# Kernel optimization log

Measured on AMD Instinct MI355X. Metric: run time of the kernel, lower is better.

The kernel has to match this reference:

```python
import jax, jax.numpy as jnp
import numpy as np

B, D_IN, D_F = 4096, 1024, 256   # batch, extractor input dim, feature dim
M, K = 10, 8                      # n_mixtures, n_components per mixture
LOG2PI = float(np.log(2.0 * np.pi))


def setup_inputs() -> dict:
    key = jax.random.key(0)
    k0, k1, k2, k3, k4 = jax.random.split(key, 5)
    x = jax.random.normal(k0, (B, D_IN), jnp.float32)
    W = jax.random.normal(k1, (D_IN, D_F), jnp.float32) / np.sqrt(D_IN)
    b = jnp.zeros((D_F,), jnp.float32)
    means = jax.random.normal(k2, (M, K, D_F), jnp.float32)
    # full covariance parameter; tril is taken in forward; +I keeps the
    # Cholesky-factor diagonal positive, as torch MultivariateNormal requires
    covs = jax.random.normal(k3, (M, K, D_F, D_F), jnp.float32) * 0.01
    covs = covs + jnp.eye(D_F, dtype=jnp.float32)
    weights = jax.random.normal(k4, (M, K), jnp.float32)
    return {"x": x, "W": W, "b": b, "means": means, "covs": covs, "weights": weights}


def reference(x, W, b, means, covs, weights):
    # extractor: Linear + ReLU -> [B, D_F]
    feats = jax.nn.relu(x @ W + b)
    # scale_tril = tril(cov) for every (mixture, component): [M, K, D_F, D_F]
    L = jnp.tril(covs)
    # diff between every feature vector and every component mean: [M, K, B, D_F]
    diff = feats[None, None, :, :] - means[:, :, None, :]
    # batched triangular solve L z = diff^T -> z: [M, K, D_F, B]
    z = jax.scipy.linalg.solve_triangular(L, jnp.swapaxes(diff, -1, -2), lower=True)
    quad = jnp.sum(z * z, axis=-2)  # Mahalanobis term: [M, K, B]
    logdet = jnp.sum(jnp.log(jnp.diagonal(L, axis1=-2, axis2=-1)), axis=-1)  # [M, K]
    logp = -0.5 * (quad + D_F * LOG2PI) - logdet[..., None]  # MVN log_prob: [M, K, B]
    # per-mixture softmax over component weights, multiply into log-probs
    w = jax.nn.softmax(weights, axis=-1)  # [M, K]
    mix = w[..., None] * logp             # [M, K, B]
    # GMM returns [B, K]; DeepGMM stacks over mixtures and transposes -> [B, M, K]
    return jnp.transpose(mix, (2, 0, 1))
```

## Files before the change

kernel.cpp:

```cpp
#include <hip/hip_runtime.h>

#define B_N 4096
#define D_IN 1024
#define D_F 256
#define MK 80
#define LOG2PI 1.8378770664093453f
#define XP_S 72

typedef float f32x4 __attribute__((ext_vector_type(4)));
typedef short bf16x8 __attribute__((ext_vector_type(8)));
typedef float float4_ __attribute__((ext_vector_type(4)));
typedef unsigned int u32x4 __attribute__((ext_vector_type(4)));
typedef unsigned short u16x8 __attribute__((ext_vector_type(8)));

__device__ __forceinline__ unsigned short f2bf(float f) {
    unsigned u = __float_as_uint(f);
    u += 0x7fffu + ((u >> 16) & 1u);
    return (unsigned short)(u >> 16);
}
__device__ __forceinline__ float bf2f(unsigned short h) {
    return __uint_as_float(((unsigned)h) << 16);
}
__device__ __forceinline__ void gload_lds16(const void* g, void* l) {
    __builtin_amdgcn_global_load_lds((const __attribute__((address_space(1))) void*)g,
                                     (__attribute__((address_space(3))) void*)l, 16, 0, 0);
}
__device__ __forceinline__ bf16x8 pack8(float4_ a, float4_ b) {
    bf16x8 r;
    r[0] = (short)f2bf(a.x); r[1] = (short)f2bf(a.y);
    r[2] = (short)f2bf(a.z); r[3] = (short)f2bf(a.w);
    r[4] = (short)f2bf(b.x); r[5] = (short)f2bf(b.y);
    r[6] = (short)f2bf(b.z); r[7] = (short)f2bf(b.w);
    return r;
}

__global__ __launch_bounds__(256) void k_pre(const float* __restrict__ W,
                                             const float* __restrict__ covs,
                                             const float* __restrict__ wts,
                                             unsigned short* __restrict__ wt,
                                             float* __restrict__ wmix,
                                             float* __restrict__ ldet,
                                             unsigned short* __restrict__ covsb,
                                             float* __restrict__ dvec) {
    int bx = blockIdx.x, tid = threadIdx.x;
    if (bx < 64) {
        __shared__ unsigned short t[64][65];
        int k0 = (bx >> 2) * 64, n0 = (bx & 3) * 64;
        int r = tid / 64, c = tid % 64;
        #pragma unroll
        for (int rr = r; rr < 64; rr += 4)
            t[rr][c] = f2bf(W[(size_t)(k0 + rr) * D_F + n0 + c]);
        __syncthreads();
        #pragma unroll
        for (int rr = r; rr < 64; rr += 4)
            wt[(size_t)(n0 + rr) * D_IN + k0 + c] = t[c][rr];
    } else if (bx < 144) {
        if (tid < 64) {
            int mk = bx - 64;
            int l = tid;
            const float* Lm = covs + (size_t)mk * D_F * D_F;
            float s = 0.0f;
            for (int i = l; i < D_F; i += 64) s += logf(Lm[(size_t)i * D_F + i]);
            for (int off = 32; off; off >>= 1) s += __shfl_down(s, off);
            if (l == 0) {
                ldet[mk] = s;
                int m = mk / 8, k = mk % 8;
                float mx = -1e30f;
                for (int j = 0; j < 8; j++) mx = fmaxf(mx, wts[m * 8 + j]);
                float sum = 0.0f;
                for (int j = 0; j < 8; j++) sum += expf(wts[m * 8 + j] - mx);
                wmix[mk] = expf(wts[m * 8 + k] - mx) / sum;
            }
        }
    } else if (bx < 224) {
        int mk = bx - 144;
        const float* Cm = covs + (size_t)mk * D_F * D_F;
        unsigned short* Cb = covsb + (size_t)mk * 10 * 4096;
        #pragma unroll
        for (int I = 1; I < 4; ++I)
            for (int K = 0; K < I; ++K) {
                int idx = (I * (I - 1)) / 2 + K;
                for (int t4 = tid; t4 < 1024; t4 += 256) {
                    int r = t4 >> 4, kq = t4 & 15;
                    float4_ v = *(const float4_*)&Cm[(size_t)(I * 64 + r) * D_F
                                                     + K * 64 + kq * 4];
                    ushort4 o;
                    o.x = f2bf(v.x); o.y = f2bf(v.y); o.z = f2bf(v.z); o.w = f2bf(v.w);
                    *(ushort4*)&Cb[(size_t)idx * 4096 + r * 64 + kq * 4] = o;
                }
            }
    } else {
        int mk = bx - 224;
        const float* Cm = covs + (size_t)mk * D_F * D_F;
        unsigned short* Cb = covsb + (size_t)mk * 10 * 4096;
        __shared__ float rl[256];
        rl[tid] = 1.0f / Cm[(size_t)tid * D_F + tid];
        __syncthreads();
        dvec[mk * 256 + tid] = rl[tid];
        #pragma unroll
        for (int I = 0; I < 4; ++I) {
            for (int t4 = tid; t4 < 1024; t4 += 256) {
                int r = t4 >> 4, kq = t4 & 15;
                float4_ v = *(const float4_*)&Cm[(size_t)(I * 64 + r) * D_F
                                                 + I * 64 + kq * 4];
                float ri = rl[I * 64 + r];
                int base = kq * 4;
                ushort4 o;
                o.x = (base     < r) ? f2bf(v.x * ri) : (unsigned short)0;
                o.y = (base + 1 < r) ? f2bf(v.y * ri) : (unsigned short)0;
                o.z = (base + 2 < r) ? f2bf(v.z * ri) : (unsigned short)0;
                o.w = (base + 3 < r) ? f2bf(v.w * ri) : (unsigned short)0;
                *(ushort4*)&Cb[(size_t)(6 + I) * 4096 + r * 64 + base] = o;
            }
        }
    }
}

__global__ __launch_bounds__(256) void k_dinv(unsigned short* __restrict__ covsb,
                                              const float* __restrict__ dvec) {
    int mk = blockIdx.x, I = blockIdx.y;
    __shared__ unsigned short X[64][XP_S];
    __shared__ unsigned short Yt[2][64][XP_S];
    __shared__ float dl[64];
    int tid = threadIdx.x, w = tid >> 6, l = tid & 63;
    unsigned short* Xg = covsb + ((size_t)mk * 10 + 6 + I) * 4096;
    for (int t = tid; t < 512; t += 256) {
        int r = t >> 3, c8 = t & 7;
        *(u16x8*)&X[r][c8 * 8] = *(const u16x8*)&Xg[r * 64 + c8 * 8];
    }
    if (tid < 64) dl[tid] = dvec[mk * 256 + I * 64 + tid];
    __syncthreads();
    for (int t = tid; t < 4096; t += 256) {
        int j = t >> 6, i = t & 63;
        unsigned short xv = X[i][j];
        Yt[0][j][i] = (i == j) ? (unsigned short)0x3F80
                               : (unsigned short)(xv ^ 0x8000u);
    }
    __syncthreads();
    int cur = 0;
    for (int it = 0; it < 3; ++it) {
        bf16x8 a0 = *(const bf16x8*)&Yt[cur][16 * w + (l & 15)][(l >> 4) * 8];
        bf16x8 a1 = *(const bf16x8*)&Yt[cur][16 * w + (l & 15)][32 + (l >> 4) * 8];
        f32x4 acc[4] = {{0, 0, 0, 0}, {0, 0, 0, 0}, {0, 0, 0, 0}, {0, 0, 0, 0}};
        #pragma unroll
        for (int ni = 0; ni < 4; ++ni) {
            bf16x8 b0 = *(const bf16x8*)&X[ni * 16 + (l & 15)][(l >> 4) * 8];
            bf16x8 b1 = *(const bf16x8*)&X[ni * 16 + (l & 15)][32 + (l >> 4) * 8];
            acc[ni] = __builtin_amdgcn_mfma_f32_16x16x32_bf16(a0, b0, acc[ni], 0, 0, 0);
            acc[ni] = __builtin_amdgcn_mfma_f32_16x16x32_bf16(a1, b1, acc[ni], 0, 0, 0);
        }
        #pragma unroll
        for (int ni = 0; ni < 4; ++ni)
            #pragma unroll
            for (int q = 0; q < 4; ++q) {
                int i = ni * 16 + (l & 15);
                int j = 16 * w + (l >> 4) * 4 + q;
                float v = ((i == j) ? 1.0f : 0.0f) - acc[ni][q];
                Yt[cur ^ 1][j][i] = f2bf(v);
            }
        __syncthreads();
        cur ^= 1;
    }
    for (int t = tid; t < 4096; t += 256) {
        int r = t >> 6, c = t & 63;
        Xg[t] = f2bf(bf2f(Yt[cur][c][r]) * dl[c]);
    }
}

__global__ __launch_bounds__(256) void k_inv_panel(
        const unsigned short* __restrict__ covsb,
        const float* __restrict__ means,
        unsigned short* __restrict__ linv,
        float* __restrict__ cpart) {
    int mk = blockIdx.x, J = blockIdx.y;
    int jc0 = J * 64;
    __shared__ unsigned short Xp[4][64][XP_S];
    __shared__ unsigned short Sb[64][XP_S];
    __shared__ float muS[64];
    int tid = threadIdx.x, w = tid >> 6, l = tid & 63;
    const unsigned short* Cb = covsb + (size_t)mk * 10 * 4096;
    const unsigned short* Dmk = Cb + 6 * 4096;
    unsigned short* Lout = linv + (size_t)mk * D_F * D_F;

    for (int t = tid; t < jc0 * 8; t += 256) {
        int r = t >> 3, s = t & 7;
        ((u32x4*)(Lout + (size_t)r * D_F + jc0))[s] = (u32x4){0, 0, 0, 0};
    }
    const unsigned short* DJ = Dmk + J * 4096;
    for (int t = tid; t < 4096; t += 256) {
        int r = t >> 6, c = t & 63;
        Xp[J][c][r] = DJ[t];
    }
    for (int t = tid; t < 512; t += 256) {
        int r = t >> 3, s = t & 7;
        ((u32x4*)(Lout + (size_t)(jc0 + r) * D_F + jc0))[s] = ((const u32x4*)(DJ + r * 64))[s];
    }
    __syncthreads();

    for (int I = J + 1; I < 4; ++I) {
        f32x4 acc[4] = {};
        for (int K = J; K < I; ++K) {
            const unsigned short* CB = Cb + (size_t)((I * (I - 1)) / 2 + K) * 4096;
            #pragma unroll
            for (int kb = 0; kb < 2; ++kb) {
                bf16x8 af = *(const bf16x8*)&Xp[K][w * 16 + (l & 15)][kb * 32 + (l >> 4) * 8];
                #pragma unroll
                for (int ni = 0; ni < 4; ++ni) {
                    bf16x8 bf = *(const bf16x8*)&CB[(size_t)(ni * 16 + (l & 15)) * 64
                                                    + kb * 32 + (l >> 4) * 8];
                    acc[ni] = __builtin_amdgcn_mfma_f32_16x16x32_bf16(af, bf, acc[ni], 0, 0, 0);
                }
            }
        }
        #pragma unroll
        for (int ni = 0; ni < 4; ++ni)
            #pragma unroll
            for (int q = 0; q < 4; ++q)
                Sb[w * 16 + ((l >> 4) << 2) + q][ni * 16 + (l & 15)] = f2bf(acc[ni][q]);
        __syncthreads();
        f32x4 acc2[4] = {};
        #pragma unroll
        for (int kb = 0; kb < 2; ++kb) {
            bf16x8 af = *(const bf16x8*)&Sb[w * 16 + (l & 15)][kb * 32 + (l >> 4) * 8];
            #pragma unroll
            for (int ni = 0; ni < 4; ++ni) {
                const u16x8* dp = (const u16x8*)(Dmk + (size_t)I * 4096
                                  + (ni * 16 + (l & 15)) * 64 + kb * 32 + (l >> 4) * 8);
                u16x8 dv = *dp ^ (unsigned short)0x8000;
                bf16x8 bf = __builtin_bit_cast(bf16x8, dv);
                acc2[ni] = __builtin_amdgcn_mfma_f32_16x16x32_bf16(af, bf, acc2[ni], 0, 0, 0);
            }
        }
        #pragma unroll
        for (int ni = 0; ni < 4; ++ni)
            #pragma unroll
            for (int q = 0; q < 4; ++q) {
                int c = w * 16 + ((l >> 4) << 2) + q;
                int r = ni * 16 + (l & 15);
                unsigned short hv = f2bf(acc2[ni][q]);
                Xp[I][c][r] = hv;
                Lout[(size_t)(I * 64 + r) * D_F + jc0 + c] = hv;
            }
        __syncthreads();
    }

    if (tid < 64) muS[tid] = means[(size_t)mk * D_F + jc0 + tid];
    __syncthreads();
    {
        int I = w, r = l;
        float s = 0.0f;
        if (I >= J) {
            for (int c = 0; c < 64; ++c)
                s += bf2f(Xp[I][c][r]) * muS[c];
        }
        cpart[((size_t)mk * 4 + J) * 256 + tid] = s;
    }
}

__global__ __launch_bounds__(256) void k_feat(const float* __restrict__ x,
                                              const unsigned short* __restrict__ wt,
                                              const float* __restrict__ bias,
                                              unsigned short* __restrict__ fb) {
    __shared__ unsigned short As[64][64];
    __shared__ unsigned short Bs[64][64];
    int b0 = blockIdx.x * 64;
    int n0 = blockIdx.y * 64;
    int tid = threadIdx.x, w = tid >> 6, l = tid & 63;
    int wm = w >> 1, wn = w & 1;
    f32x4 acc[2][2] = {};
    for (int k0 = 0; k0 < D_IN; k0 += 64) {
        float4_ av[2][2];
        #pragma unroll
        for (int it = 0; it < 2; ++it) {
            int o16 = tid + it * 256;
            int r = o16 >> 3, c = o16 & 7;
            const float* gp = x + (size_t)(b0 + r) * D_IN + k0 + c * 8;
            av[it][0] = *(const float4_*)gp;
            av[it][1] = *(const float4_*)(gp + 4);
        }
        __syncthreads();
        #pragma unroll
        for (int it = 0; it < 2; ++it) {
            int o16 = tid + it * 256;
            int r = o16 >> 3, c = o16 & 7;
            int cs = c ^ (r & 7);
            *(bf16x8*)&As[r][cs * 8] = pack8(av[it][0], av[it][1]);
            int c8 = c ^ (r & 7);
            gload_lds16(wt + (size_t)(n0 + r) * D_IN + k0 + c8 * 8, &Bs[0][0] + o16 * 8);
        }
        __syncthreads();
        #pragma unroll
        for (int ks = 0; ks < 2; ++ks) {
            int uw = ((ks * 4 + (l >> 4)) ^ (l & 7)) * 8;
            bf16x8 af[2], bg[2];
            #pragma unroll
            for (int mi = 0; mi < 2; ++mi)
                af[mi] = *(const bf16x8*)&As[wm * 32 + mi * 16 + (l & 15)][uw];
            #pragma unroll
            for (int ni = 0; ni < 2; ++ni)
                bg[ni] = *(const bf16x8*)&Bs[wn * 32 + ni * 16 + (l & 15)][uw];
            #pragma unroll
            for (int mi = 0; mi < 2; ++mi)
                #pragma unroll
                for (int ni = 0; ni < 2; ++ni)
                    acc[mi][ni] = __builtin_amdgcn_mfma_f32_16x16x32_bf16(
                        af[mi], bg[ni], acc[mi][ni], 0, 0, 0);
        }
    }
    #pragma unroll
    for (int mi = 0; mi < 2; ++mi)
        #pragma unroll
        for (int ni = 0; ni < 2; ++ni) {
            int d = n0 + wn * 32 + ni * 16 + (l & 15);
            float bia = bias[d];
            #pragma unroll
            for (int r = 0; r < 4; ++r) {
                int b = b0 + wm * 32 + mi * 16 + (l >> 4) * 4 + r;
                float v = fmaxf(acc[mi][ni][r] + bia, 0.0f);
                fb[(size_t)b * D_F + d] = f2bf(v);
            }
        }
}

__global__ __launch_bounds__(512) void k_gmm(const unsigned short* __restrict__ linv,
                                             const unsigned short* __restrict__ fb,
                                             const float* __restrict__ cpart,
                                             const float* __restrict__ wmix,
                                             const float* __restrict__ ldet,
                                             float* __restrict__ out) {
    __shared__ unsigned short As[256][64];
    __shared__ unsigned short Bs[128][64];
    __shared__ float cb[D_F];
    __shared__ float qpart[4][128];
    int mk = blockIdx.x;
    int b0 = blockIdx.y * 128;
    int tid = threadIdx.x, w = tid >> 6, l = tid & 63;
    int wm = w >> 1, wn = w & 1;
    const unsigned short* Ab = linv + (size_t)mk * D_F * D_F;
    if (tid < D_F) {
        const float* cp = cpart + (size_t)mk * 4 * D_F + tid;
        cb[tid] = cp[0] + cp[256] + cp[512] + cp[768];
    }
    f32x4 acc[4][4] = {};
    for (int k0 = 0; k0 < D_F; k0 += 64) {
        #pragma unroll
        for (int it = 0; it < 4; ++it) {
            int o16 = tid + it * 512;
            int r = o16 >> 3, c8 = (o16 & 7) ^ (r & 7);
            gload_lds16(Ab + (size_t)r * D_F + k0 + c8 * 8, &As[0][0] + o16 * 8);
        }
        #pragma unroll
        for (int it = 0; it < 2; ++it) {
            int o16 = tid + it * 512;
            int r = o16 >> 3, c8 = (o16 & 7) ^ (r & 7);
            gload_lds16(fb + (size_t)(b0 + r) * D_F + k0 + c8 * 8, &Bs[0][0] + o16 * 8);
        }
        __syncthreads();
        #pragma unroll
        for (int ks = 0; ks < 2; ++ks) {
            int uw = ((ks * 4 + (l >> 4)) ^ (l & 7)) * 8;
            bf16x8 af[4], bg[4];
            #pragma unroll
            for (int mi = 0; mi < 4; ++mi)
                af[mi] = *(const bf16x8*)&As[wm * 64 + mi * 16 + (l & 15)][uw];
            #pragma unroll
            for (int ni = 0; ni < 4; ++ni)
                bg[ni] = *(const bf16x8*)&Bs[wn * 64 + ni * 16 + (l & 15)][uw];
            #pragma unroll
            for (int mi = 0; mi < 4; ++mi)
                #pragma unroll
                for (int ni = 0; ni < 4; ++ni)
                    acc[mi][ni] = __builtin_amdgcn_mfma_f32_16x16x32_bf16(
                        af[mi], bg[ni], acc[mi][ni], 0, 0, 0);
        }
        __syncthreads();
    }
    float p[4] = {0, 0, 0, 0};
    #pragma unroll
    for (int mi = 0; mi < 4; ++mi) {
        int ibase = wm * 64 + mi * 16 + ((l >> 4) << 2);
        #pragma unroll
        for (int r = 0; r < 4; ++r) {
            float cv = cb[ibase + r];
            #pragma unroll
            for (int ni = 0; ni < 4; ++ni) {
                float z = acc[mi][ni][r] - cv;
                p[ni] += z * z;
            }
        }
    }
    #pragma unroll
    for (int ni = 0; ni < 4; ++ni) {
        p[ni] += __shfl_xor(p[ni], 16);
        p[ni] += __shfl_xor(p[ni], 32);
    }
    if (l < 16) {
        #pragma unroll
        for (int ni = 0; ni < 4; ++ni)
            qpart[wm][wn * 64 + ni * 16 + l] = p[ni];
    }
    __syncthreads();
    if (tid < 128) {
        float q = qpart[0][tid] + qpart[1][tid] + qpart[2][tid] + qpart[3][tid];
        float lp = -0.5f * (q + (float)D_F * LOG2PI) - ldet[mk];
        out[(size_t)(b0 + tid) * MK + mk] = wmix[mk] * lp;
    }
}

extern "C" void kernel_launch(void* const* d_in, const int* in_sizes, int n_in,
                              void* d_out, int out_size, void* d_ws, size_t ws_size,
                              hipStream_t stream) {
    const float* x     = (const float*)d_in[0];
    const float* W     = (const float*)d_in[1];
    const float* bias  = (const float*)d_in[2];
    const float* means = (const float*)d_in[3];
    const float* covs  = (const float*)d_in[4];
    const float* wts   = (const float*)d_in[5];
    float* out = (float*)d_out;

    char* ws = (char*)d_ws;
    unsigned short* covsb = (unsigned short*)(ws);
    unsigned short* wt    = (unsigned short*)(ws + 6553600);
    unsigned short* fb    = (unsigned short*)(ws + 7077888);
    unsigned short* linv  = (unsigned short*)(ws + 9175040);
    float* dvec = (float*)(ws + 19660800);
    float* wmix = (float*)(ws + 19742720);
    float* ldet = (float*)(ws + 19743040);
    float* cpart = (float*)(ws + 6553600);

    k_pre<<<dim3(304), dim3(256), 0, stream>>>(W, covs, wts, wt, wmix, ldet, covsb, dvec);
    k_dinv<<<dim3(MK, 4), dim3(256), 0, stream>>>(covsb, dvec);
    k_feat<<<dim3(64, 4), dim3(256), 0, stream>>>(x, wt, bias, fb);
    k_inv_panel<<<dim3(MK, 4), dim3(256), 0, stream>>>(covsb, means, linv, cpart);
    k_gmm<<<dim3(MK, 32), dim3(512), 0, stream>>>(linv, fb, cpart, wmix, ldet, out);
}
```

Measured before the change: 89.70 us.

## Replace blocked triangular inverse with fixed-point iteration, drop k_dinv kernel

Row-scales the whole lower-triangular covariance by the inverse diagonal during preprocessing and merges the two k_pre branches into one. The separate diagonal-block inversion kernel and the panel forward-substitution are replaced by a single k_linv kernel. It runs five Jacobi/Neumann-style sweeps T <- I - N*T over the block column, with each wave owning one row block and double-buffered shared memory. This removes a kernel launch and the serial per-block dependency chain, at the cost of more MFMA work per iteration. Whether five sweeps give enough accuracy depends on the 256x256 strictly-lower part being nilpotent in 4 block steps plus the intra-block error.

```diff
diff --git a/kernel.cpp b/kernel.cpp
--- a/kernel.cpp
+++ b/kernel.cpp
@@ -72,31 +72,29 @@
                 wmix[mk] = expf(wts[m * 8 + k] - mx) / sum;
             }
         }
-    } else if (bx < 224) {
+    } else {
         int mk = bx - 144;
         const float* Cm = covs + (size_t)mk * D_F * D_F;
         unsigned short* Cb = covsb + (size_t)mk * 10 * 4096;
+        __shared__ float rl[256];
+        rl[tid] = 1.0f / Cm[(size_t)tid * D_F + tid];
+        __syncthreads();
+        dvec[mk * 256 + tid] = rl[tid];
         #pragma unroll
         for (int I = 1; I < 4; ++I)
             for (int K = 0; K < I; ++K) {
                 int idx = (I * (I - 1)) / 2 + K;
                 for (int t4 = tid; t4 < 1024; t4 += 256) {
                     int r = t4 >> 4, kq = t4 & 15;
+                    float ri = rl[I * 64 + r];
                     float4_ v = *(const float4_*)&Cm[(size_t)(I * 64 + r) * D_F
                                                      + K * 64 + kq * 4];
                     ushort4 o;
-                    o.x = f2bf(v.x); o.y = f2bf(v.y); o.z = f2bf(v.z); o.w = f2bf(v.w);
+                    o.x = f2bf(v.x * ri); o.y = f2bf(v.y * ri);
+                    o.z = f2bf(v.z * ri); o.w = f2bf(v.w * ri);
                     *(ushort4*)&Cb[(size_t)idx * 4096 + r * 64 + kq * 4] = o;
                 }
             }
-    } else {
-        int mk = bx - 224;
-        const float* Cm = covs + (size_t)mk * D_F * D_F;
-        unsigned short* Cb = covsb + (size_t)mk * 10 * 4096;
-        __shared__ float rl[256];
-        rl[tid] = 1.0f / Cm[(size_t)tid * D_F + tid];
-        __syncthreads();
-        dvec[mk * 256 + tid] = rl[tid];
         #pragma unroll
         for (int I = 0; I < 4; ++I) {
             for (int t4 = tid; t4 < 1024; t4 += 256) {
@@ -116,144 +114,105 @@
     }
 }
 
-__global__ __launch_bounds__(256) void k_dinv(unsigned short* __restrict__ covsb,
-                                              const float* __restrict__ dvec) {
-    int mk = blockIdx.x, I = blockIdx.y;
-    __shared__ unsigned short X[64][XP_S];
-    __shared__ unsigned short Yt[2][64][XP_S];
-    __shared__ float dl[64];
-    int tid = threadIdx.x, w = tid >> 6, l = tid & 63;
-    unsigned short* Xg = covsb + ((size_t)mk * 10 + 6 + I) * 4096;
-    for (int t = tid; t < 512; t += 256) {
-        int r = t >> 3, c8 = t & 7;
-        *(u16x8*)&X[r][c8 * 8] = *(const u16x8*)&Xg[r * 64 + c8 * 8];
-    }
-    if (tid < 64) dl[tid] = dvec[mk * 256 + I * 64 + tid];
-    __syncthreads();
-    for (int t = tid; t < 4096; t += 256) {
-        int j = t >> 6, i = t & 63;
-        unsigned short xv = X[i][j];
-        Yt[0][j][i] = (i == j) ? (unsigned short)0x3F80
-                               : (unsigned short)(xv ^ 0x8000u);
-    }
-    __syncthreads();
-    int cur = 0;
-    for (int it = 0; it < 3; ++it) {
-        bf16x8 a0 = *(const bf16x8*)&Yt[cur][16 * w + (l & 15)][(l >> 4) * 8];
-        bf16x8 a1 = *(const bf16x8*)&Yt[cur][16 * w + (l & 15)][32 + (l >> 4) * 8];
-        f32x4 acc[4] = {{0, 0, 0, 0}, {0, 0, 0, 0}, {0, 0, 0, 0}, {0, 0, 0, 0}};
-        #pragma unroll
-        for (int ni = 0; ni < 4; ++ni) {
-            bf16x8 b0 = *(const bf16x8*)&X[ni * 16 + (l & 15)][(l >> 4) * 8];
-            bf16x8 b1 = *(const bf16x8*)&X[ni * 16 + (l & 15)][32 + (l >> 4) * 8];
-            acc[ni] = __builtin_amdgcn_mfma_f32_16x16x32_bf16(a0, b0, acc[ni], 0, 0, 0);
-            acc[ni] = __builtin_amdgcn_mfma_f32_16x16x32_bf16(a1, b1, acc[ni], 0, 0, 0);
-        }
-        #pragma unroll
-        for (int ni = 0; ni < 4; ++ni)
-            #pragma unroll
-            for (int q = 0; q < 4; ++q) {
-                int i = ni * 16 + (l & 15);
-                int j = 16 * w + (l >> 4) * 4 + q;
-                float v = ((i == j) ? 1.0f : 0.0f) - acc[ni][q];
-                Yt[cur ^ 1][j][i] = f2bf(v);
-            }
-        __syncthreads();
-        cur ^= 1;
-    }
-    for (int t = tid; t < 4096; t += 256) {
-        int r = t >> 6, c = t & 63;
-        Xg[t] = f2bf(bf2f(Yt[cur][c][r]) * dl[c]);
-    }
-}
-
-__global__ __launch_bounds__(256) void k_inv_panel(
+__global__ __launch_bounds__(256) void k_linv(
         const unsigned short* __restrict__ covsb,
+        const float* __restrict__ dvec,
         const float* __restrict__ means,
         unsigned short* __restrict__ linv,
         float* __restrict__ cpart) {
     int mk = blockIdx.x, J = blockIdx.y;
     int jc0 = J * 64;
-    __shared__ unsigned short Xp[4][64][XP_S];
-    __shared__ unsigned short Sb[64][XP_S];
+    __shared__ unsigned short Tt[2][4][64][XP_S];
+    __shared__ float rd[64];
     __shared__ float muS[64];
     int tid = threadIdx.x, w = tid >> 6, l = tid & 63;
     const unsigned short* Cb = covsb + (size_t)mk * 10 * 4096;
-    const unsigned short* Dmk = Cb + 6 * 4096;
     unsigned short* Lout = linv + (size_t)mk * D_F * D_F;
 
+    if (tid < 64) {
+        rd[tid] = dvec[mk * 256 + jc0 + tid];
+        muS[tid] = means[(size_t)mk * D_F + jc0 + tid];
+    }
     for (int t = tid; t < jc0 * 8; t += 256) {
         int r = t >> 3, s = t & 7;
         ((u32x4*)(Lout + (size_t)r * D_F + jc0))[s] = (u32x4){0, 0, 0, 0};
     }
-    const unsigned short* DJ = Dmk + J * 4096;
-    for (int t = tid; t < 4096; t += 256) {
-        int r = t >> 6, c = t & 63;
-        Xp[J][c][r] = DJ[t];
-    }
-    for (int t = tid; t < 512; t += 256) {
-        int r = t >> 3, s = t & 7;
-        ((u32x4*)(Lout + (size_t)(jc0 + r) * D_F + jc0))[s] = ((const u32x4*)(DJ + r * 64))[s];
+    {
+        u16x8* p = (u16x8*)&Tt[0][0][0][0];
+        u16x8 z = {0, 0, 0, 0, 0, 0, 0, 0};
+        for (int t = tid; t < (4 * 64 * XP_S) / 8; t += 256) p[t] = z;
     }
     __syncthreads();
-
-    for (int I = J + 1; I < 4; ++I) {
-        f32x4 acc[4] = {};
-        for (int K = J; K < I; ++K) {
-            const unsigned short* CB = Cb + (size_t)((I * (I - 1)) / 2 + K) * 4096;
-            #pragma unroll
-            for (int kb = 0; kb < 2; ++kb) {
-                bf16x8 af = *(const bf16x8*)&Xp[K][w * 16 + (l & 15)][kb * 32 + (l >> 4) * 8];
-                #pragma unroll
-                for (int ni = 0; ni < 4; ++ni) {
-                    bf16x8 bf = *(const bf16x8*)&CB[(size_t)(ni * 16 + (l & 15)) * 64
-                                                    + kb * 32 + (l >> 4) * 8];
-                    acc[ni] = __builtin_amdgcn_mfma_f32_16x16x32_bf16(af, bf, acc[ni], 0, 0, 0);
+    if (tid < 64) Tt[0][J][tid][tid] = 0x3F80;
+    __syncthreads();
+
+    int cur = 0;
+    int I = w;
+    for (int s = 0; s < 5; ++s) {
+        if (I >= J) {
+            f32x4 acc[4][4] = {};
+            for (int K = J; K <= I; ++K) {
+                const unsigned short* XB =
+                    Cb + (size_t)((K < I) ? (I * (I - 1)) / 2 + K : 6 + I) * 4096;
+                #pragma unroll
+                for (int kb = 0; kb < 2; ++kb) {
+                    bf16x8 bfv[4];
+                    #pragma unroll
+                    for (int ni = 0; ni < 4; ++ni)
+                        bfv[ni] = *(const bf16x8*)&Tt[cur][K][ni * 16 + (l & 15)]
+                                                     [kb * 32 + (l >> 4) * 8];
+                    #pragma unroll
+                    for (int mi = 0; mi < 4; ++mi) {
+                        bf16x8 afv = *(const bf16x8*)&XB[(size_t)(mi * 16 + (l & 15)) * 64
+                                                         + kb * 32 + (l >> 4) * 8];
+                        #pragma unroll
+                        for (int ni = 0; ni < 4; ++ni)
+                            acc[mi][ni] = __builtin_amdgcn_mfma_f32_16x16x32_bf16(
+                                afv, bfv[ni], acc[mi][ni], 0, 0, 0);
+                    }
                 }
             }
-        }
-        #pragma unroll
-        for (int ni = 0; ni < 4; ++ni)
-            #pragma unroll
-            for (int q = 0; q < 4; ++q)
-                Sb[w * 16 + ((l >> 4) << 2) + q][ni * 16 + (l & 15)] = f2bf(acc[ni][q]);
-        __syncthreads();
-        f32x4 acc2[4] = {};
-        #pragma unroll
-        for (int kb = 0; kb < 2; ++kb) {
-            bf16x8 af = *(const bf16x8*)&Sb[w * 16 + (l & 15)][kb * 32 + (l >> 4) * 8];
-            #pragma unroll
-            for (int ni = 0; ni < 4; ++ni) {
-                const u16x8* dp = (const u16x8*)(Dmk + (size_t)I * 4096
-                                  + (ni * 16 + (l & 15)) * 64 + kb * 32 + (l >> 4) * 8);
-                u16x8 dv = *dp ^ (unsigned short)0x8000;
-                bf16x8 bf = __builtin_bit_cast(bf16x8, dv);
-                acc2[ni] = __builtin_amdgcn_mfma_f32_16x16x32_bf16(af, bf, acc2[ni], 0, 0, 0);
-            }
-        }
-        #pragma unroll
-        for (int ni = 0; ni < 4; ++ni)
-            #pragma unroll
-            for (int q = 0; q < 4; ++q) {
-                int c = w * 16 + ((l >> 4) << 2) + q;
-                int r = ni * 16 + (l & 15);
-                unsigned short hv = f2bf(acc2[ni][q]);
-                Xp[I][c][r] = hv;
-                Lout[(size_t)(I * 64 + r) * D_F + jc0 + c] = hv;
-            }
-        __syncthreads();
-    }
-
-    if (tid < 64) muS[tid] = means[(size_t)mk * D_F + jc0 + tid];
-    __syncthreads();
+            if (s < 4) {
+                #pragma unroll
+                for (int mi = 0; mi < 4; ++mi)
+                    #pragma unroll
+                    for (int ni = 0; ni < 4; ++ni)
+                        #pragma unroll
+                        for (int q = 0; q < 4; ++q) {
+                            int m = mi * 16 + (l >> 4) * 4 + q;
+                            int n = ni * 16 + (l & 15);
+                            float v = ((I == J && m == n) ? 1.0f : 0.0f) - acc[mi][ni][q];
+                            Tt[cur ^ 1][I][n][m] = f2bf(v);
+                        }
+            } else {
+                #pragma unroll
+                for (int mi = 0; mi < 4; ++mi)
+                    #pragma unroll
+                    for (int ni = 0; ni < 4; ++ni) {
+                        int n = ni * 16 + (l & 15);
+                        float rdv = rd[n];
+                        #pragma unroll
+                        for (int q = 0; q < 4; ++q) {
+                            int m = mi * 16 + (l >> 4) * 4 + q;
+                            float v = (((I == J && m == n) ? 1.0f : 0.0f)
+                                       - acc[mi][ni][q]) * rdv;
+                            unsigned short hv = f2bf(v);
+                            Tt[cur ^ 1][I][n][m] = hv;
+                            Lout[(size_t)(I * 64 + m) * D_F + jc0 + n] = hv;
+                        }
+                    }
+            }
+        }
+        __syncthreads();
+        cur ^= 1;
+    }
     {
-        int I = w, r = l;
-        float s = 0.0f;
+        float ssum = 0.0f;
         if (I >= J) {
             for (int c = 0; c < 64; ++c)
-                s += bf2f(Xp[I][c][r]) * muS[c];
-        }
-        cpart[((size_t)mk * 4 + J) * 256 + tid] = s;
+                ssum += bf2f(Tt[cur][I][c][l]) * muS[c];
+        }
+        cpart[((size_t)mk * 4 + J) * 256 + tid] = ssum;
     }
 }
 
@@ -428,9 +387,8 @@
     float* ldet = (float*)(ws + 19743040);
     float* cpart = (float*)(ws + 6553600);
 
-    k_pre<<<dim3(304), dim3(256), 0, stream>>>(W, covs, wts, wt, wmix, ldet, covsb, dvec);
-    k_dinv<<<dim3(MK, 4), dim3(256), 0, stream>>>(covsb, dvec);
+    k_pre<<<dim3(224), dim3(256), 0, stream>>>(W, covs, wts, wt, wmix, ldet, covsb, dvec);
     k_feat<<<dim3(64, 4), dim3(256), 0, stream>>>(x, wt, bias, fb);
-    k_inv_panel<<<dim3(MK, 4), dim3(256), 0, stream>>>(covsb, means, linv, cpart);
+    k_linv<<<dim3(MK, 4), dim3(256), 0, stream>>>(covsb, dvec, means, linv, cpart);
     k_gmm<<<dim3(MK, 32), dim3(512), 0, stream>>>(linv, fb, cpart, wmix, ldet, out);
 }
```

Result: slower. 99.66 us (+11.1%).

## Fuse diagonal-block inversion into preprocessing kernel and widen feature GEMM K-tile

Applied to the files above, without the earlier changes.

Merges the separate diagonal-block inverse kernel into k_pre. Each (mixture-component, block) pair now gets its own workgroup that builds the scaled strict-lower block directly in LDS, inverts it with MFMA iterations and writes it out, which removes one launch and the global round trip through covsb and dvec. The feature GEMM also doubles its K step from 64 to 128, halving the number of barrier-separated iterations at the cost of more LDS and registers per block. k_pre now has a larger shared-memory footprint for all of its branches, which may lower its occupancy.

```diff
diff --git a/kernel.cpp b/kernel.cpp
--- a/kernel.cpp
+++ b/kernel.cpp
@@ -40,8 +40,7 @@
                                              unsigned short* __restrict__ wt,
                                              float* __restrict__ wmix,
                                              float* __restrict__ ldet,
-                                             unsigned short* __restrict__ covsb,
-                                             float* __restrict__ dvec) {
+                                             unsigned short* __restrict__ covsb) {
     int bx = blockIdx.x, tid = threadIdx.x;
     if (bx < 64) {
         __shared__ unsigned short t[64][65];
@@ -90,80 +89,65 @@
                 }
             }
     } else {
-        int mk = bx - 224;
+        int b = bx - 224;
+        int mk = b >> 2, I = b & 3;
+        int i0 = I * 64;
+        __shared__ float rl[64];
+        __shared__ unsigned short X[64][XP_S];
+        __shared__ unsigned short Yt[2][64][XP_S];
+        int w = tid >> 6, l = tid & 63;
         const float* Cm = covs + (size_t)mk * D_F * D_F;
-        unsigned short* Cb = covsb + (size_t)mk * 10 * 4096;
-        __shared__ float rl[256];
-        rl[tid] = 1.0f / Cm[(size_t)tid * D_F + tid];
-        __syncthreads();
-        dvec[mk * 256 + tid] = rl[tid];
-        #pragma unroll
-        for (int I = 0; I < 4; ++I) {
-            for (int t4 = tid; t4 < 1024; t4 += 256) {
-                int r = t4 >> 4, kq = t4 & 15;
-                float4_ v = *(const float4_*)&Cm[(size_t)(I * 64 + r) * D_F
-                                                 + I * 64 + kq * 4];
-                float ri = rl[I * 64 + r];
-                int base = kq * 4;
-                ushort4 o;
-                o.x = (base     < r) ? f2bf(v.x * ri) : (unsigned short)0;
-                o.y = (base + 1 < r) ? f2bf(v.y * ri) : (unsigned short)0;
-                o.z = (base + 2 < r) ? f2bf(v.z * ri) : (unsigned short)0;
-                o.w = (base + 3 < r) ? f2bf(v.w * ri) : (unsigned short)0;
-                *(ushort4*)&Cb[(size_t)(6 + I) * 4096 + r * 64 + base] = o;
-            }
-        }
-    }
-}
-
-__global__ __launch_bounds__(256) void k_dinv(unsigned short* __restrict__ covsb,
-                                              const float* __restrict__ dvec) {
-    int mk = blockIdx.x, I = blockIdx.y;
-    __shared__ unsigned short X[64][XP_S];
-    __shared__ unsigned short Yt[2][64][XP_S];
-    __shared__ float dl[64];
-    int tid = threadIdx.x, w = tid >> 6, l = tid & 63;
-    unsigned short* Xg = covsb + ((size_t)mk * 10 + 6 + I) * 4096;
-    for (int t = tid; t < 512; t += 256) {
-        int r = t >> 3, c8 = t & 7;
-        *(u16x8*)&X[r][c8 * 8] = *(const u16x8*)&Xg[r * 64 + c8 * 8];
-    }
-    if (tid < 64) dl[tid] = dvec[mk * 256 + I * 64 + tid];
-    __syncthreads();
-    for (int t = tid; t < 4096; t += 256) {
-        int j = t >> 6, i = t & 63;
-        unsigned short xv = X[i][j];
-        Yt[0][j][i] = (i == j) ? (unsigned short)0x3F80
-                               : (unsigned short)(xv ^ 0x8000u);
-    }
-    __syncthreads();
-    int cur = 0;
-    for (int it = 0; it < 3; ++it) {
-        bf16x8 a0 = *(const bf16x8*)&Yt[cur][16 * w + (l & 15)][(l >> 4) * 8];
-        bf16x8 a1 = *(const bf16x8*)&Yt[cur][16 * w + (l & 15)][32 + (l >> 4) * 8];
-        f32x4 acc[4] = {{0, 0, 0, 0}, {0, 0, 0, 0}, {0, 0, 0, 0}, {0, 0, 0, 0}};
-        #pragma unroll
-        for (int ni = 0; ni < 4; ++ni) {
-            bf16x8 b0 = *(const bf16x8*)&X[ni * 16 + (l & 15)][(l >> 4) * 8];
-            bf16x8 b1 = *(const bf16x8*)&X[ni * 16 + (l & 15)][32 + (l >> 4) * 8];
-            acc[ni] = __builtin_amdgcn_mfma_f32_16x16x32_bf16(a0, b0, acc[ni], 0, 0, 0);
-            acc[ni] = __builtin_amdgcn_mfma_f32_16x16x32_bf16(a1, b1, acc[ni], 0, 0, 0);
-        }
-        #pragma unroll
-        for (int ni = 0; ni < 4; ++ni)
-            #pragma unroll
-            for (int q = 0; q < 4; ++q) {
-                int i = ni * 16 + (l & 15);
-                int j = 16 * w + (l >> 4) * 4 + q;
-                float v = ((i == j) ? 1.0f : 0.0f) - acc[ni][q];
-                Yt[cur ^ 1][j][i] = f2bf(v);
-            }
-        __syncthreads();
-        cur ^= 1;
-    }
-    for (int t = tid; t < 4096; t += 256) {
-        int r = t >> 6, c = t & 63;
-        Xg[t] = f2bf(bf2f(Yt[cur][c][r]) * dl[c]);
+        if (tid < 64) rl[tid] = 1.0f / Cm[(size_t)(i0 + tid) * D_F + i0 + tid];
+        __syncthreads();
+        for (int t4 = tid; t4 < 1024; t4 += 256) {
+            int r = t4 >> 4, kq = t4 & 15;
+            float4_ v = *(const float4_*)&Cm[(size_t)(i0 + r) * D_F + i0 + kq * 4];
+            float ri = rl[r];
+            int base = kq * 4;
+            ushort4 o;
+            o.x = (base     < r) ? f2bf(v.x * ri) : (unsigned short)0;
+            o.y = (base + 1 < r) ? f2bf(v.y * ri) : (unsigned short)0;
+            o.z = (base + 2 < r) ? f2bf(v.z * ri) : (unsigned short)0;
+            o.w = (base + 3 < r) ? f2bf(v.w * ri) : (unsigned short)0;
+            *(ushort4*)&X[r][base] = o;
+        }
+        __syncthreads();
+        for (int t = tid; t < 4096; t += 256) {
+            int j = t >> 6, i = t & 63;
+            unsigned short xv = X[i][j];
+            Yt[0][j][i] = (i == j) ? (unsigned short)0x3F80
+                                   : (unsigned short)(xv ^ 0x8000u);
+        }
+        __syncthreads();
+        int cur = 0;
+        for (int it = 0; it < 3; ++it) {
+            bf16x8 a0 = *(const bf16x8*)&Yt[cur][16 * w + (l & 15)][(l >> 4) * 8];
+            bf16x8 a1 = *(const bf16x8*)&Yt[cur][16 * w + (l & 15)][32 + (l >> 4) * 8];
+            f32x4 acc[4] = {{0, 0, 0, 0}, {0, 0, 0, 0}, {0, 0, 0, 0}, {0, 0, 0, 0}};
+            #pragma unroll
+            for (int ni = 0; ni < 4; ++ni) {
+                bf16x8 b0 = *(const bf16x8*)&X[ni * 16 + (l & 15)][(l >> 4) * 8];
+                bf16x8 b1 = *(const bf16x8*)&X[ni * 16 + (l & 15)][32 + (l >> 4) * 8];
+                acc[ni] = __builtin_amdgcn_mfma_f32_16x16x32_bf16(a0, b0, acc[ni], 0, 0, 0);
+                acc[ni] = __builtin_amdgcn_mfma_f32_16x16x32_bf16(a1, b1, acc[ni], 0, 0, 0);
+            }
+            #pragma unroll
+            for (int ni = 0; ni < 4; ++ni)
+                #pragma unroll
+                for (int q = 0; q < 4; ++q) {
+                    int i = ni * 16 + (l & 15);
+                    int j = 16 * w + (l >> 4) * 4 + q;
+                    float v = ((i == j) ? 1.0f : 0.0f) - acc[ni][q];
+                    Yt[cur ^ 1][j][i] = f2bf(v);
+                }
+            __syncthreads();
+            cur ^= 1;
+        }
+        unsigned short* Xg = covsb + ((size_t)mk * 10 + 6 + I) * 4096;
+        for (int t = tid; t < 4096; t += 256) {
+            int r = t >> 6, c = t & 63;
+            Xg[t] = f2bf(bf2f(Yt[cur][c][r]) * rl[c]);
+        }
     }
 }
 
@@ -261,36 +245,35 @@
                                               const unsigned short* __restrict__ wt,
                                               const float* __restrict__ bias,
                                               unsigned short* __restrict__ fb) {
-    __shared__ unsigned short As[64][64];
-    __shared__ unsigned short Bs[64][64];
+    __shared__ unsigned short As[64][128];
+    __shared__ unsigned short Bs[64][128];
     int b0 = blockIdx.x * 64;
     int n0 = blockIdx.y * 64;
     int tid = threadIdx.x, w = tid >> 6, l = tid & 63;
     int wm = w >> 1, wn = w & 1;
     f32x4 acc[2][2] = {};
-    for (int k0 = 0; k0 < D_IN; k0 += 64) {
-        float4_ av[2][2];
-        #pragma unroll
-        for (int it = 0; it < 2; ++it) {
+    for (int k0 = 0; k0 < D_IN; k0 += 128) {
+        float4_ av[4][2];
+        #pragma unroll
+        for (int it = 0; it < 4; ++it) {
             int o16 = tid + it * 256;
-            int r = o16 >> 3, c = o16 & 7;
+            int r = o16 >> 4, c = o16 & 15;
             const float* gp = x + (size_t)(b0 + r) * D_IN + k0 + c * 8;
             av[it][0] = *(const float4_*)gp;
             av[it][1] = *(const float4_*)(gp + 4);
         }
         __syncthreads();
         #pragma unroll
-        for (int it = 0; it < 2; ++it) {
+        for (int it = 0; it < 4; ++it) {
             int o16 = tid + it * 256;
-            int r = o16 >> 3, c = o16 & 7;
+            int r = o16 >> 4, c = o16 & 15;
             int cs = c ^ (r & 7);
             *(bf16x8*)&As[r][cs * 8] = pack8(av[it][0], av[it][1]);
-            int c8 = c ^ (r & 7);
-            gload_lds16(wt + (size_t)(n0 + r) * D_IN + k0 + c8 * 8, &Bs[0][0] + o16 * 8);
-        }
-        __syncthreads();
-        #pragma unroll
-        for (int ks = 0; ks < 2; ++ks) {
+            gload_lds16(wt + (size_t)(n0 + r) * D_IN + k0 + cs * 8, &Bs[0][0] + o16 * 8);
+        }
+        __syncthreads();
+        #pragma unroll
+        for (int ks = 0; ks < 4; ++ks) {
             int uw = ((ks * 4 + (l >> 4)) ^ (l & 7)) * 8;
             bf16x8 af[2], bg[2];
             #pragma unroll
@@ -423,13 +406,11 @@
     unsigned short* wt    = (unsigned short*)(ws + 6553600);
     unsigned short* fb    = (unsigned short*)(ws + 7077888);
     unsigned short* linv  = (unsigned short*)(ws + 9175040);
-    float* dvec = (float*)(ws + 19660800);
     float* wmix = (float*)(ws + 19742720);
     float* ldet = (float*)(ws + 19743040);
     float* cpart = (float*)(ws + 6553600);
 
-    k_pre<<<dim3(304), dim3(256), 0, stream>>>(W, covs, wts, wt, wmix, ldet, covsb, dvec);
-    k_dinv<<<dim3(MK, 4), dim3(256), 0, stream>>>(covsb, dvec);
+    k_pre<<<dim3(544), dim3(256), 0, stream>>>(W, covs, wts, wt, wmix, ldet, covsb);
     k_feat<<<dim3(64, 4), dim3(256), 0, stream>>>(x, wt, bias, fb);
     k_inv_panel<<<dim3(MK, 4), dim3(256), 0, stream>>>(covsb, means, linv, cpart);
     k_gmm<<<dim3(MK, 32), dim3(512), 0, stream>>>(linv, fb, cpart, wmix, ldet, out);
```

After: 82.90 us. 7.6% less time.
